# Performance work log

Hardware: AMD Instinct MI355X
Metric: run time of the kernel (lower is better)

The kernel has to match this reference:

```python
import jax, jax.numpy as jnp
import numpy as np

B = 65536  # batch size


def setup_inputs() -> dict:
    key = jax.random.key(0)
    ks = jax.random.split(key, 8)
    x = jax.random.normal(ks[0], (B, 784), dtype=jnp.float32)
    conv_w = jax.random.normal(ks[1], (3, 3), dtype=jnp.float32)
    w1 = jax.random.normal(ks[2], (676, 256), dtype=jnp.float32) * 0.04
    b1 = jnp.zeros((256,), dtype=jnp.float32)
    w2 = jax.random.normal(ks[3], (256, 128), dtype=jnp.float32) * 0.06
    b2 = jnp.zeros((128,), dtype=jnp.float32)
    w3 = jax.random.normal(ks[4], (128, 10), dtype=jnp.float32) * 0.09
    b3 = jnp.zeros((10,), dtype=jnp.float32)
    return {"x": x, "conv_w": conv_w, "w1": w1, "b1": b1,
            "w2": w2, "b2": b2, "w3": w3, "b3": b3}


def reference(x, conv_w, w1, b1, w2, b2, w3, b3):
    # x: [B, 784] -> images [B, 1, 28, 28]
    img = x.reshape(-1, 1, 28, 28)
    # Convolve() is a valid cross-correlation (tensordot of window with kernel,
    # no flip) -> lax.conv_general_dilated (also no kernel flip).
    kern = conv_w.reshape(1, 1, 3, 3)  # [O, I, kh, kw]
    y = jax.lax.conv_general_dilated(
        img, kern, window_strides=(1, 1), padding="VALID",
        dimension_numbers=("NCHW", "OIHW", "NCHW"))  # [B, 1, 26, 26]
    h = y.reshape(y.shape[0], 26 * 26)
    h = jax.nn.relu(h @ w1 + b1)
    h = jax.nn.relu(h @ w2 + b2)
    return h @ w3 + b3  # [B, 10] logits
```

## Files before the change

kernel.cpp:

```cpp
#include <hip/hip_runtime.h>
#include <hip/hip_bf16.h>

typedef __bf16 bf16x8 __attribute__((ext_vector_type(8)));
typedef float  f32x4  __attribute__((ext_vector_type(4)));

#define B_ROWS 65536
#define MR 32
#define H0S 712
#define H1S 264
#define H2S 136
#define KC1 22
#define KC2 8
#define KC3 4

#define W1B_ELEMS (704*256)
#define W2B_ELEMS (256*128)
#define W3B_ELEMS (128*16)

__global__ void pack_weights(const float* __restrict__ w1,
                             const float* __restrict__ w2,
                             const float* __restrict__ w3,
                             __hip_bfloat16* __restrict__ w1b,
                             __hip_bfloat16* __restrict__ w2b,
                             __hip_bfloat16* __restrict__ w3b) {
    int idx = blockIdx.x * 256 + threadIdx.x;
    if (idx < W1B_ELEMS) {
        int ki = idx & 31, t = idx >> 5;
        int n = t & 255, kc = t >> 8;
        int k = kc * 32 + ki;
        float v = (k < 676) ? w1[k * 256 + n] : 0.0f;
        w1b[idx] = __float2bfloat16(v);
    } else if (idx < W1B_ELEMS + W2B_ELEMS) {
        int j = idx - W1B_ELEMS;
        int ki = j & 31, t = j >> 5;
        int n = t & 127, kc = t >> 7;
        w2b[j] = __float2bfloat16(w2[(kc * 32 + ki) * 128 + n]);
    } else if (idx < W1B_ELEMS + W2B_ELEMS + W3B_ELEMS) {
        int j = idx - W1B_ELEMS - W2B_ELEMS;
        int ki = j & 31, t = j >> 5;
        int n = t & 15, kc = t >> 4;
        float v = (n < 10) ? w3[(kc * 32 + ki) * 10 + n] : 0.0f;
        w3b[j] = __float2bfloat16(v);
    }
}

__global__ __launch_bounds__(256, 2)
void fused_model(const float* __restrict__ x, const float* __restrict__ cw,
                 const __hip_bfloat16* __restrict__ w1b, const float* __restrict__ b1,
                 const __hip_bfloat16* __restrict__ w2b, const float* __restrict__ b2,
                 const __hip_bfloat16* __restrict__ w3b, const float* __restrict__ b3,
                 float* __restrict__ out) {
    __shared__ __align__(16) char smem[MR * H0S * 2 + MR * H1S * 2];
    __hip_bfloat16* h0s = (__hip_bfloat16*)smem;
    __hip_bfloat16* h1s = (__hip_bfloat16*)(smem + MR * H0S * 2);
    __hip_bfloat16* h2s = (__hip_bfloat16*)smem;

    const int tid = threadIdx.x;
    const int r0  = blockIdx.x * MR;

    const float c00 = cw[0], c01 = cw[1], c02 = cw[2];
    const float c10 = cw[3], c11 = cw[4], c12 = cw[5];
    const float c20 = cw[6], c21 = cw[7], c22 = cw[8];

    for (int t = tid; t < MR * 26; t += 256) {
        int r = t / 26;
        int i = t - r * 26;
        const float* xr = x + (size_t)(r0 + r) * 784 + i * 28;
        float acc[26];
        #pragma unroll
        for (int j = 0; j < 26; j++) acc[j] = 0.0f;
        #pragma unroll
        for (int di = 0; di < 3; di++) {
            float rb[28];
            const float4* p4 = (const float4*)(xr + di * 28);
            #pragma unroll
            for (int q = 0; q < 7; q++) {
                float4 v = p4[q];
                rb[q*4+0] = v.x; rb[q*4+1] = v.y; rb[q*4+2] = v.z; rb[q*4+3] = v.w;
            }
            const float k0 = (di == 0) ? c00 : ((di == 1) ? c10 : c20);
            const float k1 = (di == 0) ? c01 : ((di == 1) ? c11 : c21);
            const float k2 = (di == 0) ? c02 : ((di == 1) ? c12 : c22);
            #pragma unroll
            for (int j = 0; j < 26; j++)
                acc[j] += k0 * rb[j] + k1 * rb[j+1] + k2 * rb[j+2];
        }
        __hip_bfloat16* hp = h0s + r * H0S + i * 26;
        #pragma unroll
        for (int j = 0; j < 26; j++) hp[j] = __float2bfloat16(acc[j]);
    }
    for (int t = tid; t < MR * 36; t += 256) {
        int r = t / 36;
        int c = 676 + (t - r * 36);
        h0s[r * H0S + c] = __float2bfloat16(0.0f);
    }
    __syncthreads();

    const int wave = tid >> 6;
    const int lane = tid & 63;
    const int l15  = lane & 15;
    const int g    = lane >> 4;

    {
        f32x4 acc[2][4];
        #pragma unroll
        for (int mt = 0; mt < 2; mt++)
            #pragma unroll
            for (int nt = 0; nt < 4; nt++)
                acc[mt][nt] = (f32x4){0.f, 0.f, 0.f, 0.f};
        const int nb = wave * 64;
        for (int kc = 0; kc < KC1; kc++) {
            bf16x8 a[2], b[4];
            #pragma unroll
            for (int mt = 0; mt < 2; mt++)
                a[mt] = *(const bf16x8*)(h0s + (mt * 16 + l15) * H0S + kc * 32 + g * 8);
            #pragma unroll
            for (int nt = 0; nt < 4; nt++)
                b[nt] = *(const bf16x8*)(w1b + ((kc * 256 + nb + nt * 16 + l15) * 32 + g * 8));
            #pragma unroll
            for (int mt = 0; mt < 2; mt++)
                #pragma unroll
                for (int nt = 0; nt < 4; nt++)
                    acc[mt][nt] = __builtin_amdgcn_mfma_f32_16x16x32_bf16(
                        a[mt], b[nt], acc[mt][nt], 0, 0, 0);
        }
        #pragma unroll
        for (int nt = 0; nt < 4; nt++) {
            const int n = nb + nt * 16 + l15;
            const float bias = b1[n];
            #pragma unroll
            for (int mt = 0; mt < 2; mt++) {
                #pragma unroll
                for (int q = 0; q < 4; q++) {
                    const int row = mt * 16 + g * 4 + q;
                    float v = acc[mt][nt][q] + bias;
                    h1s[row * H1S + n] = __float2bfloat16(fmaxf(v, 0.0f));
                }
            }
        }
    }
    __syncthreads();

    {
        f32x4 acc[2][2];
        #pragma unroll
        for (int mt = 0; mt < 2; mt++)
            #pragma unroll
            for (int nt = 0; nt < 2; nt++)
                acc[mt][nt] = (f32x4){0.f, 0.f, 0.f, 0.f};
        const int nb = wave * 32;
        for (int kc = 0; kc < KC2; kc++) {
            bf16x8 a[2], b[2];
            #pragma unroll
            for (int mt = 0; mt < 2; mt++)
                a[mt] = *(const bf16x8*)(h1s + (mt * 16 + l15) * H1S + kc * 32 + g * 8);
            #pragma unroll
            for (int nt = 0; nt < 2; nt++)
                b[nt] = *(const bf16x8*)(w2b + ((kc * 128 + nb + nt * 16 + l15) * 32 + g * 8));
            #pragma unroll
            for (int mt = 0; mt < 2; mt++)
                #pragma unroll
                for (int nt = 0; nt < 2; nt++)
                    acc[mt][nt] = __builtin_amdgcn_mfma_f32_16x16x32_bf16(
                        a[mt], b[nt], acc[mt][nt], 0, 0, 0);
        }
        #pragma unroll
        for (int nt = 0; nt < 2; nt++) {
            const int n = nb + nt * 16 + l15;
            const float bias = b2[n];
            #pragma unroll
            for (int mt = 0; mt < 2; mt++) {
                #pragma unroll
                for (int q = 0; q < 4; q++) {
                    const int row = mt * 16 + g * 4 + q;
                    float v = acc[mt][nt][q] + bias;
                    h2s[row * H2S + n] = __float2bfloat16(fmaxf(v, 0.0f));
                }
            }
        }
    }
    __syncthreads();

    if (wave < 2) {
        f32x4 acc3 = (f32x4){0.f, 0.f, 0.f, 0.f};
        for (int kc = 0; kc < KC3; kc++) {
            bf16x8 a = *(const bf16x8*)(h2s + (wave * 16 + l15) * H2S + kc * 32 + g * 8);
            bf16x8 b = *(const bf16x8*)(w3b + ((kc * 16 + l15) * 32 + g * 8));
            acc3 = __builtin_amdgcn_mfma_f32_16x16x32_bf16(a, b, acc3, 0, 0, 0);
        }
        if (l15 < 10) {
            const float bias = b3[l15];
            #pragma unroll
            for (int q = 0; q < 4; q++) {
                const int row = wave * 16 + g * 4 + q;
                out[(size_t)(r0 + row) * 10 + l15] = acc3[q] + bias;
            }
        }
    }
}

extern "C" void kernel_launch(void* const* d_in, const int* in_sizes, int n_in,
                              void* d_out, int out_size, void* d_ws, size_t ws_size,
                              hipStream_t stream) {
    const float* x  = (const float*)d_in[0];
    const float* cw = (const float*)d_in[1];
    const float* w1 = (const float*)d_in[2];
    const float* b1 = (const float*)d_in[3];
    const float* w2 = (const float*)d_in[4];
    const float* b2 = (const float*)d_in[5];
    const float* w3 = (const float*)d_in[6];
    const float* b3 = (const float*)d_in[7];
    float* out = (float*)d_out;

    __hip_bfloat16* w1b = (__hip_bfloat16*)d_ws;
    __hip_bfloat16* w2b = w1b + W1B_ELEMS;
    __hip_bfloat16* w3b = w2b + W2B_ELEMS;

    const int pack_total = W1B_ELEMS + W2B_ELEMS + W3B_ELEMS;
    pack_weights<<<(pack_total + 255) / 256, 256, 0, stream>>>(w1, w2, w3, w1b, w2b, w3b);
    fused_model<<<B_ROWS / MR, 256, 0, stream>>>(x, cw, w1b, b1, w2b, b2, w3b, b3, out);
}
```

Baseline: 360.8 us.

## Halve rows per block, raise occupancy, and restructure conv into paired bf16 stores

Cuts rows per block from 32 to 16 and raises the launch-bounds occupancy hint to 4 blocks per CU, which shrinks shared memory and accumulator registers per block. The goal is more resident waves to hide the global loads of x and the weights. The conv stage now loads all three input rows first and writes outputs as packed bf16 pairs, and the padding is zeroed with 32-bit stores. The cost is that each weight fragment loaded from global memory now feeds half as many MFMAs, so weight traffic per output row doubles.

```diff
diff --git a/kernel.cpp b/kernel.cpp
--- a/kernel.cpp
+++ b/kernel.cpp
@@ -5,7 +5,7 @@
 typedef float  f32x4  __attribute__((ext_vector_type(4)));
 
 #define B_ROWS 65536
-#define MR 32
+#define MR 16
 #define H0S 712
 #define H1S 264
 #define H2S 136
@@ -44,7 +44,7 @@
     }
 }
 
-__global__ __launch_bounds__(256, 2)
+__global__ __launch_bounds__(256, 4)
 void fused_model(const float* __restrict__ x, const float* __restrict__ cw,
                  const __hip_bfloat16* __restrict__ w1b, const float* __restrict__ b1,
                  const __hip_bfloat16* __restrict__ w2b, const float* __restrict__ b2,
@@ -66,33 +66,37 @@
         int r = t / 26;
         int i = t - r * 26;
         const float* xr = x + (size_t)(r0 + r) * 784 + i * 28;
-        float acc[26];
-        #pragma unroll
-        for (int j = 0; j < 26; j++) acc[j] = 0.0f;
+        float rb[3][28];
         #pragma unroll
         for (int di = 0; di < 3; di++) {
-            float rb[28];
             const float4* p4 = (const float4*)(xr + di * 28);
             #pragma unroll
             for (int q = 0; q < 7; q++) {
                 float4 v = p4[q];
-                rb[q*4+0] = v.x; rb[q*4+1] = v.y; rb[q*4+2] = v.z; rb[q*4+3] = v.w;
-            }
-            const float k0 = (di == 0) ? c00 : ((di == 1) ? c10 : c20);
-            const float k1 = (di == 0) ? c01 : ((di == 1) ? c11 : c21);
-            const float k2 = (di == 0) ? c02 : ((di == 1) ? c12 : c22);
-            #pragma unroll
-            for (int j = 0; j < 26; j++)
-                acc[j] += k0 * rb[j] + k1 * rb[j+1] + k2 * rb[j+2];
-        }
-        __hip_bfloat16* hp = h0s + r * H0S + i * 26;
-        #pragma unroll
-        for (int j = 0; j < 26; j++) hp[j] = __float2bfloat16(acc[j]);
-    }
-    for (int t = tid; t < MR * 36; t += 256) {
-        int r = t / 36;
-        int c = 676 + (t - r * 36);
-        h0s[r * H0S + c] = __float2bfloat16(0.0f);
+                rb[di][q*4+0] = v.x; rb[di][q*4+1] = v.y;
+                rb[di][q*4+2] = v.z; rb[di][q*4+3] = v.w;
+            }
+        }
+        __hip_bfloat162* hp = (__hip_bfloat162*)(h0s + r * H0S + i * 26);
+        #pragma unroll
+        for (int k = 0; k < 13; k++) {
+            const int j0 = 2 * k, j1 = 2 * k + 1;
+            float a0 = c00*rb[0][j0] + c01*rb[0][j0+1] + c02*rb[0][j0+2]
+                     + c10*rb[1][j0] + c11*rb[1][j0+1] + c12*rb[1][j0+2]
+                     + c20*rb[2][j0] + c21*rb[2][j0+1] + c22*rb[2][j0+2];
+            float a1 = c00*rb[0][j1] + c01*rb[0][j1+1] + c02*rb[0][j1+2]
+                     + c10*rb[1][j1] + c11*rb[1][j1+1] + c12*rb[1][j1+2]
+                     + c20*rb[2][j1] + c21*rb[2][j1+1] + c22*rb[2][j1+2];
+            __hip_bfloat162 pr;
+            pr.x = __float2bfloat16(a0);
+            pr.y = __float2bfloat16(a1);
+            hp[k] = pr;
+        }
+    }
+    for (int t = tid; t < MR * 18; t += 256) {
+        int r = t / 18;
+        int c = t - r * 18;
+        ((uint*)(h0s + r * H0S + 676))[c] = 0u;
     }
     __syncthreads();
 
@@ -102,89 +106,69 @@
     const int g    = lane >> 4;
 
     {
-        f32x4 acc[2][4];
-        #pragma unroll
-        for (int mt = 0; mt < 2; mt++)
-            #pragma unroll
-            for (int nt = 0; nt < 4; nt++)
-                acc[mt][nt] = (f32x4){0.f, 0.f, 0.f, 0.f};
+        f32x4 acc[4];
+        #pragma unroll
+        for (int nt = 0; nt < 4; nt++)
+            acc[nt] = (f32x4){0.f, 0.f, 0.f, 0.f};
         const int nb = wave * 64;
         for (int kc = 0; kc < KC1; kc++) {
-            bf16x8 a[2], b[4];
-            #pragma unroll
-            for (int mt = 0; mt < 2; mt++)
-                a[mt] = *(const bf16x8*)(h0s + (mt * 16 + l15) * H0S + kc * 32 + g * 8);
+            bf16x8 a = *(const bf16x8*)(h0s + l15 * H0S + kc * 32 + g * 8);
+            bf16x8 b[4];
             #pragma unroll
             for (int nt = 0; nt < 4; nt++)
                 b[nt] = *(const bf16x8*)(w1b + ((kc * 256 + nb + nt * 16 + l15) * 32 + g * 8));
             #pragma unroll
-            for (int mt = 0; mt < 2; mt++)
-                #pragma unroll
-                for (int nt = 0; nt < 4; nt++)
-                    acc[mt][nt] = __builtin_amdgcn_mfma_f32_16x16x32_bf16(
-                        a[mt], b[nt], acc[mt][nt], 0, 0, 0);
+            for (int nt = 0; nt < 4; nt++)
+                acc[nt] = __builtin_amdgcn_mfma_f32_16x16x32_bf16(a, b[nt], acc[nt], 0, 0, 0);
         }
         #pragma unroll
         for (int nt = 0; nt < 4; nt++) {
             const int n = nb + nt * 16 + l15;
             const float bias = b1[n];
             #pragma unroll
-            for (int mt = 0; mt < 2; mt++) {
-                #pragma unroll
-                for (int q = 0; q < 4; q++) {
-                    const int row = mt * 16 + g * 4 + q;
-                    float v = acc[mt][nt][q] + bias;
-                    h1s[row * H1S + n] = __float2bfloat16(fmaxf(v, 0.0f));
-                }
+            for (int q = 0; q < 4; q++) {
+                const int row = g * 4 + q;
+                float v = acc[nt][q] + bias;
+                h1s[row * H1S + n] = __float2bfloat16(fmaxf(v, 0.0f));
             }
         }
     }
     __syncthreads();
 
     {
-        f32x4 acc[2][2];
-        #pragma unroll
-        for (int mt = 0; mt < 2; mt++)
-            #pragma unroll
-            for (int nt = 0; nt < 2; nt++)
-                acc[mt][nt] = (f32x4){0.f, 0.f, 0.f, 0.f};
+        f32x4 acc[2];
+        #pragma unroll
+        for (int nt = 0; nt < 2; nt++)
+            acc[nt] = (f32x4){0.f, 0.f, 0.f, 0.f};
         const int nb = wave * 32;
         for (int kc = 0; kc < KC2; kc++) {
-            bf16x8 a[2], b[2];
-            #pragma unroll
-            for (int mt = 0; mt < 2; mt++)
-                a[mt] = *(const bf16x8*)(h1s + (mt * 16 + l15) * H1S + kc * 32 + g * 8);
+            bf16x8 a = *(const bf16x8*)(h1s + l15 * H1S + kc * 32 + g * 8);
+            bf16x8 b[2];
             #pragma unroll
             for (int nt = 0; nt < 2; nt++)
                 b[nt] = *(const bf16x8*)(w2b + ((kc * 128 + nb + nt * 16 + l15) * 32 + g * 8));
             #pragma unroll
-            for (int mt = 0; mt < 2; mt++)
-                #pragma unroll
-                for (int nt = 0; nt < 2; nt++)
-                    acc[mt][nt] = __builtin_amdgcn_mfma_f32_16x16x32_bf16(
-                        a[mt], b[nt], acc[mt][nt], 0, 0, 0);
+            for (int nt = 0; nt < 2; nt++)
+                acc[nt] = __builtin_amdgcn_mfma_f32_16x16x32_bf16(a, b[nt], acc[nt], 0, 0, 0);
         }
         #pragma unroll
         for (int nt = 0; nt < 2; nt++) {
             const int n = nb + nt * 16 + l15;
             const float bias = b2[n];
             #pragma unroll
-            for (int mt = 0; mt < 2; mt++) {
-                #pragma unroll
-                for (int q = 0; q < 4; q++) {
-                    const int row = mt * 16 + g * 4 + q;
-                    float v = acc[mt][nt][q] + bias;
-                    h2s[row * H2S + n] = __float2bfloat16(fmaxf(v, 0.0f));
-                }
+            for (int q = 0; q < 4; q++) {
+                const int row = g * 4 + q;
+                float v = acc[nt][q] + bias;
+                h2s[row * H2S + n] = __float2bfloat16(fmaxf(v, 0.0f));
             }
         }
     }
     __syncthreads();
 
-    if (wave < 2) {
+    if (wave == 0) {
         f32x4 acc3 = (f32x4){0.f, 0.f, 0.f, 0.f};
         for (int kc = 0; kc < KC3; kc++) {
-            bf16x8 a = *(const bf16x8*)(h2s + (wave * 16 + l15) * H2S + kc * 32 + g * 8);
+            bf16x8 a = *(const bf16x8*)(h2s + l15 * H2S + kc * 32 + g * 8);
             bf16x8 b = *(const bf16x8*)(w3b + ((kc * 16 + l15) * 32 + g * 8));
             acc3 = __builtin_amdgcn_mfma_f32_16x16x32_bf16(a, b, acc3, 0, 0, 0);
         }
@@ -192,7 +176,7 @@
             const float bias = b3[l15];
             #pragma unroll
             for (int q = 0; q < 4; q++) {
-                const int row = wave * 16 + g * 4 + q;
+                const int row = g * 4 + q;
                 out[(size_t)(r0 + row) * 10 + l15] = acc3[q] + bias;
             }
         }
```

Result: slower. 408.3 us (+13.2%).

## Batch conv input loads and software-pipeline MFMA operand loads in GEMM loops

Applied to the files above, without the earlier changes.

The conv stage now issues all 21 float4 global loads for a row triple up front, using an empty asm barrier to keep them together, and then computes two outputs per step and stores them as packed bf16x2. The pad zeroing uses 32-bit stores. The layer-1 and layer-2 GEMM loops are fully unrolled with a 3-deep register ring that prefetches A and B operands two k-chunks ahead to hide LDS and global latency behind the MFMAs. This raises register pressure under launch_bounds(256,2) and could cause spills or lower occupancy.

```diff
diff --git a/kernel.cpp b/kernel.cpp
--- a/kernel.cpp
+++ b/kernel.cpp
@@ -66,33 +66,45 @@
         int r = t / 26;
         int i = t - r * 26;
         const float* xr = x + (size_t)(r0 + r) * 784 + i * 28;
-        float acc[26];
-        #pragma unroll
-        for (int j = 0; j < 26; j++) acc[j] = 0.0f;
+        float4 v[21];
         #pragma unroll
         for (int di = 0; di < 3; di++) {
-            float rb[28];
             const float4* p4 = (const float4*)(xr + di * 28);
             #pragma unroll
+            for (int q = 0; q < 7; q++) v[di * 7 + q] = p4[q];
+        }
+        #pragma unroll
+        for (int k = 0; k < 21; k++)
+            asm volatile("" :: "v"(v[k].x), "v"(v[k].y), "v"(v[k].z), "v"(v[k].w));
+        float rb[3][28];
+        #pragma unroll
+        for (int di = 0; di < 3; di++) {
+            #pragma unroll
             for (int q = 0; q < 7; q++) {
-                float4 v = p4[q];
-                rb[q*4+0] = v.x; rb[q*4+1] = v.y; rb[q*4+2] = v.z; rb[q*4+3] = v.w;
-            }
-            const float k0 = (di == 0) ? c00 : ((di == 1) ? c10 : c20);
-            const float k1 = (di == 0) ? c01 : ((di == 1) ? c11 : c21);
-            const float k2 = (di == 0) ? c02 : ((di == 1) ? c12 : c22);
-            #pragma unroll
-            for (int j = 0; j < 26; j++)
-                acc[j] += k0 * rb[j] + k1 * rb[j+1] + k2 * rb[j+2];
-        }
-        __hip_bfloat16* hp = h0s + r * H0S + i * 26;
-        #pragma unroll
-        for (int j = 0; j < 26; j++) hp[j] = __float2bfloat16(acc[j]);
-    }
-    for (int t = tid; t < MR * 36; t += 256) {
-        int r = t / 36;
-        int c = 676 + (t - r * 36);
-        h0s[r * H0S + c] = __float2bfloat16(0.0f);
+                rb[di][q*4+0] = v[di*7+q].x; rb[di][q*4+1] = v[di*7+q].y;
+                rb[di][q*4+2] = v[di*7+q].z; rb[di][q*4+3] = v[di*7+q].w;
+            }
+        }
+        __hip_bfloat162* hp = (__hip_bfloat162*)(h0s + r * H0S + i * 26);
+        #pragma unroll
+        for (int k = 0; k < 13; k++) {
+            const int j0 = 2 * k, j1 = 2 * k + 1;
+            float a0 = c00*rb[0][j0] + c01*rb[0][j0+1] + c02*rb[0][j0+2]
+                     + c10*rb[1][j0] + c11*rb[1][j0+1] + c12*rb[1][j0+2]
+                     + c20*rb[2][j0] + c21*rb[2][j0+1] + c22*rb[2][j0+2];
+            float a1 = c00*rb[0][j1] + c01*rb[0][j1+1] + c02*rb[0][j1+2]
+                     + c10*rb[1][j1] + c11*rb[1][j1+1] + c12*rb[1][j1+2]
+                     + c20*rb[2][j1] + c21*rb[2][j1+1] + c22*rb[2][j1+2];
+            __hip_bfloat162 pr;
+            pr.x = __float2bfloat16(a0);
+            pr.y = __float2bfloat16(a1);
+            hp[k] = pr;
+        }
+    }
+    for (int t = tid; t < MR * 18; t += 256) {
+        int r = t / 18;
+        int c = t - r * 18;
+        ((uint*)(h0s + r * H0S + 676))[c] = 0u;
     }
     __syncthreads();
 
@@ -109,20 +121,34 @@
             for (int nt = 0; nt < 4; nt++)
                 acc[mt][nt] = (f32x4){0.f, 0.f, 0.f, 0.f};
         const int nb = wave * 64;
+        bf16x8 ab[3][2], bb[3][4];
+        #pragma unroll
+        for (int p = 0; p < 2; p++) {
+            #pragma unroll
+            for (int mt = 0; mt < 2; mt++)
+                ab[p][mt] = *(const bf16x8*)(h0s + (mt * 16 + l15) * H0S + p * 32 + g * 8);
+            #pragma unroll
+            for (int nt = 0; nt < 4; nt++)
+                bb[p][nt] = *(const bf16x8*)(w1b + ((p * 256 + nb + nt * 16 + l15) * 32 + g * 8));
+        }
+        #pragma unroll
         for (int kc = 0; kc < KC1; kc++) {
-            bf16x8 a[2], b[4];
-            #pragma unroll
-            for (int mt = 0; mt < 2; mt++)
-                a[mt] = *(const bf16x8*)(h0s + (mt * 16 + l15) * H0S + kc * 32 + g * 8);
-            #pragma unroll
-            for (int nt = 0; nt < 4; nt++)
-                b[nt] = *(const bf16x8*)(w1b + ((kc * 256 + nb + nt * 16 + l15) * 32 + g * 8));
+            const int cur = kc % 3;
+            const int nxt = (kc + 2) % 3;
+            if (kc + 2 < KC1) {
+                #pragma unroll
+                for (int mt = 0; mt < 2; mt++)
+                    ab[nxt][mt] = *(const bf16x8*)(h0s + (mt * 16 + l15) * H0S + (kc + 2) * 32 + g * 8);
+                #pragma unroll
+                for (int nt = 0; nt < 4; nt++)
+                    bb[nxt][nt] = *(const bf16x8*)(w1b + (((kc + 2) * 256 + nb + nt * 16 + l15) * 32 + g * 8));
+            }
             #pragma unroll
             for (int mt = 0; mt < 2; mt++)
                 #pragma unroll
                 for (int nt = 0; nt < 4; nt++)
                     acc[mt][nt] = __builtin_amdgcn_mfma_f32_16x16x32_bf16(
-                        a[mt], b[nt], acc[mt][nt], 0, 0, 0);
+                        ab[cur][mt], bb[cur][nt], acc[mt][nt], 0, 0, 0);
         }
         #pragma unroll
         for (int nt = 0; nt < 4; nt++) {
@@ -149,20 +175,34 @@
             for (int nt = 0; nt < 2; nt++)
                 acc[mt][nt] = (f32x4){0.f, 0.f, 0.f, 0.f};
         const int nb = wave * 32;
+        bf16x8 ab[3][2], bb[3][2];
+        #pragma unroll
+        for (int p = 0; p < 2; p++) {
+            #pragma unroll
+            for (int mt = 0; mt < 2; mt++)
+                ab[p][mt] = *(const bf16x8*)(h1s + (mt * 16 + l15) * H1S + p * 32 + g * 8);
+            #pragma unroll
+            for (int nt = 0; nt < 2; nt++)
+                bb[p][nt] = *(const bf16x8*)(w2b + ((p * 128 + nb + nt * 16 + l15) * 32 + g * 8));
+        }
+        #pragma unroll
         for (int kc = 0; kc < KC2; kc++) {
-            bf16x8 a[2], b[2];
-            #pragma unroll
-            for (int mt = 0; mt < 2; mt++)
-                a[mt] = *(const bf16x8*)(h1s + (mt * 16 + l15) * H1S + kc * 32 + g * 8);
-            #pragma unroll
-            for (int nt = 0; nt < 2; nt++)
-                b[nt] = *(const bf16x8*)(w2b + ((kc * 128 + nb + nt * 16 + l15) * 32 + g * 8));
+            const int cur = kc % 3;
+            const int nxt = (kc + 2) % 3;
+            if (kc + 2 < KC2) {
+                #pragma unroll
+                for (int mt = 0; mt < 2; mt++)
+                    ab[nxt][mt] = *(const bf16x8*)(h1s + (mt * 16 + l15) * H1S + (kc + 2) * 32 + g * 8);
+                #pragma unroll
+                for (int nt = 0; nt < 2; nt++)
+                    bb[nxt][nt] = *(const bf16x8*)(w2b + (((kc + 2) * 128 + nb + nt * 16 + l15) * 32 + g * 8));
+            }
             #pragma unroll
             for (int mt = 0; mt < 2; mt++)
                 #pragma unroll
                 for (int nt = 0; nt < 2; nt++)
                     acc[mt][nt] = __builtin_amdgcn_mfma_f32_16x16x32_bf16(
-                        a[mt], b[nt], acc[mt][nt], 0, 0, 0);
+                        ab[cur][mt], bb[cur][nt], acc[mt][nt], 0, 0, 0);
         }
         #pragma unroll
         for (int nt = 0; nt < 2; nt++) {
@@ -183,6 +223,7 @@
 
     if (wave < 2) {
         f32x4 acc3 = (f32x4){0.f, 0.f, 0.f, 0.f};
+        #pragma unroll
         for (int kc = 0; kc < KC3; kc++) {
             bf16x8 a = *(const bf16x8*)(h2s + (wave * 16 + l15) * H2S + kc * 32 + g * 8);
             bf16x8 b = *(const bf16x8*)(w3b + ((kc * 16 + l15) * 32 + g * 8));
```

Result: faster. 338.9 us (-6.1%).
